# Optimization experiments

Hardware: AMD Instinct MI355X
Metric: run time of the kernel (lower is better)

## Reference

```python
import jax, jax.numpy as jnp
import numpy as np

N_NODES = 100000
N_EDGES = 1600000
N_GRAPHS = 256
D_IN = 128
D_HID = 128
D_OUT = 10
N_GIN_LAYERS = 4  # num_layers - 1
BN_EPS = 1e-5


def setup_inputs() -> dict:
    key = jax.random.key(0)
    ks = jax.random.split(key, 16)
    x = jax.random.normal(ks[0], (N_NODES, D_IN), dtype=jnp.float32)
    edge_src = jax.random.randint(ks[1], (N_EDGES,), 0, N_NODES)
    edge_dst = jax.random.randint(ks[2], (N_EDGES,), 0, N_NODES)
    graph_ids = jnp.sort(jax.random.randint(ks[3], (N_NODES,), 0, N_GRAPHS))
    s = 1.0 / np.sqrt(D_HID)
    # stacked per-layer params (all layers 128->128 since input_dim == hidden_dim)
    W1 = jax.random.normal(ks[4], (N_GIN_LAYERS, D_HID, D_HID), dtype=jnp.float32) * s
    b1 = jnp.zeros((N_GIN_LAYERS, D_HID), dtype=jnp.float32)
    g1 = jnp.ones((N_GIN_LAYERS, D_HID), dtype=jnp.float32)
    bt1 = jnp.zeros((N_GIN_LAYERS, D_HID), dtype=jnp.float32)
    W2 = jax.random.normal(ks[5], (N_GIN_LAYERS, D_HID, D_HID), dtype=jnp.float32) * s
    b2 = jnp.zeros((N_GIN_LAYERS, D_HID), dtype=jnp.float32)
    g2 = jnp.ones((N_GIN_LAYERS, D_HID), dtype=jnp.float32)
    bt2 = jnp.zeros((N_GIN_LAYERS, D_HID), dtype=jnp.float32)
    eps = jnp.zeros((N_GIN_LAYERS,), dtype=jnp.float32)          # learn_eps params
    fusion_w = jnp.ones((N_GIN_LAYERS,), dtype=jnp.float32)      # self.weight
    Wp = jax.random.normal(ks[6], (D_HID, D_OUT), dtype=jnp.float32) * s
    bp = jnp.zeros((D_OUT,), dtype=jnp.float32)
    return {"x": x, "edge_src": edge_src, "edge_dst": edge_dst, "graph_ids": graph_ids,
            "eps": eps, "fusion_w": fusion_w, "W1": W1, "b1": b1, "g1": g1, "bt1": bt1,
            "W2": W2, "b2": b2, "g2": g2, "bt2": bt2, "Wp": Wp, "bp": bp}


def _batchnorm(h, gamma, beta):
    # training-mode BatchNorm1d over node axis
    m = jnp.mean(h, axis=0)
    v = jnp.var(h, axis=0)
    return (h - m) * jax.lax.rsqrt(v + BN_EPS) * gamma + beta


def reference(x, edge_src, edge_dst, graph_ids, eps, fusion_w,
              W1, b1, g1, bt1, W2, b2, g2, bt2, Wp, bp):
    h = x
    hiddens = []
    for l in range(N_GIN_LAYERS):
        # sum neighbor aggregation (spmm with learn_eps -> no self loops in Adj)
        pooled = jax.ops.segment_sum(h[edge_src], edge_dst, num_segments=N_NODES)
        pooled = pooled + (1.0 + eps[l]) * h
        # 2-layer MLP: Linear -> BN -> ReLU -> Linear
        t = jax.nn.relu(_batchnorm(pooled @ W1[l] + b1[l], g1[l], bt1[l]))
        t = t @ W2[l] + b2[l]
        # outer BatchNorm + ReLU
        h = jax.nn.relu(_batchnorm(t, g2[l], bt2[l]))
        hiddens.append(h)
    # attention_global, attention_type == 'weight': weighted sum of 4 hidden scales
    fused = (fusion_w[0] * hiddens[0] + fusion_w[1] * hiddens[1]
             + fusion_w[2] * hiddens[2] + fusion_w[3] * hiddens[3])
    # graph sum pooling (graph_pool spmm) then final linear (dropout = eval identity)
    pooled_g = jax.ops.segment_sum(fused, graph_ids, num_segments=N_GRAPHS)
    return pooled_g @ Wp + bp
```

## Files before the change

kernel.cpp:

```cpp
#include <hip/hip_runtime.h>

#define D 128
#define DOUT 10
#define CT_STRIDE 152

typedef float f32x4 __attribute__((ext_vector_type(4)));
typedef __bf16 bf16x8 __attribute__((ext_vector_type(8)));
typedef unsigned short u16;

__device__ __forceinline__ float bf2f(u16 u) {
    return __uint_as_float(((unsigned int)u) << 16);
}
__device__ __forceinline__ u16 f2bf(float f) {
    unsigned int u = __float_as_uint(f);
    u += 0x7fffu + ((u >> 16) & 1u);
    return (u16)(u >> 16);
}

__global__ void k_zero(float4* __restrict__ p, int n4) {
    int i = blockIdx.x * 256 + threadIdx.x;
    if (i < n4) p[i] = make_float4(0.f, 0.f, 0.f, 0.f);
}

__global__ __launch_bounds__(256) void k_prepw(const float* __restrict__ W1,
                                               const float* __restrict__ W2,
                                               bf16x8* __restrict__ wswz, int L) {
    int b = blockIdx.x >> 3;
    const float* W = (b < L) ? (W1 + (size_t)b * D * D)
                             : (W2 + (size_t)(b - L) * D * D);
    bf16x8* o = wswz + (size_t)b * 2048;
    int idx = ((blockIdx.x & 7) << 8) + threadIdx.x;
    int lane_s = idx & 63;
    int f = idx >> 6;
    int n = ((f >> 2) << 4) | (lane_s & 15);
    int kb = ((f & 3) << 5) | ((lane_s >> 4) << 3);
    bf16x8 fr;
#pragma unroll
    for (int j = 0; j < 8; ++j) fr[j] = (__bf16)W[(kb + j) * D + n];
    o[idx] = fr;
}

__global__ __launch_bounds__(256) void k_hist(const int* __restrict__ dst,
                                              int* __restrict__ cnts, int E, int nb) {
    __shared__ int hist[1024];
    int tid = threadIdx.x;
    for (int i = tid; i < nb; i += 256) hist[i] = 0;
    __syncthreads();
    int e0 = blockIdx.x << 11;
    int e1 = e0 + 2048; if (e1 > E) e1 = E;
    for (int e = e0 + tid; e < e1; e += 256) atomicAdd(&hist[dst[e] >> 7], 1);
    __syncthreads();
    for (int i = tid; i < nb; i += 256) cnts[(blockIdx.x << 10) + i] = hist[i];
}

__global__ __launch_bounds__(256) void k_off(int* __restrict__ cnts,
                                             int* __restrict__ btot,
                                             int nbk, int nb) {
    int wave = threadIdx.x >> 6, lane = threadIdx.x & 63;
    int b = blockIdx.x * 4 + wave;
    if (b >= nb) return;
    int carry = 0;
    for (int base = 0; base < nbk; base += 64) {
        int idx = base + lane;
        int orig = (idx < nbk) ? cnts[(idx << 10) + b] : 0;
        int c = orig;
#pragma unroll
        for (int off = 1; off < 64; off <<= 1) {
            int v = __shfl_up(c, off);
            if (lane >= off) c += v;
        }
        if (idx < nbk) cnts[(idx << 10) + b] = carry + (c - orig);
        carry += __shfl(c, 63);
    }
    if (lane == 0) btot[b] = carry;
}

__global__ __launch_bounds__(256) void k_scat(const int* __restrict__ src,
                                              const int* __restrict__ dst,
                                              const int* __restrict__ cnts,
                                              int* __restrict__ pairs, int E, int nb) {
    __shared__ int lbase[1024];
    __shared__ int lcur[1024];
    int tid = threadIdx.x;
    for (int i = tid; i < nb; i += 256) {
        lbase[i] = cnts[(blockIdx.x << 10) + i];
        lcur[i] = 0;
    }
    __syncthreads();
    int e0 = blockIdx.x << 11;
    int e1 = e0 + 2048; if (e1 > E) e1 = E;
    for (int e = e0 + tid; e < e1; e += 256) {
        int d = dst[e];
        int b = d >> 7;
        int pos = lbase[b] + atomicAdd(&lcur[b], 1);
        if (pos < 4096) pairs[(b << 12) + pos] = (src[e] << 7) | (d & 127);
    }
}

__global__ void k_cvt(const float* __restrict__ x, u16* __restrict__ o,
                      int M, int Mpad) {
    long e = ((long)blockIdx.x * 256 + threadIdx.x) * 4;
    if (e >= (long)Mpad * D) return;
    ushort4 r;
    if (e < (long)M * D) {
        float4 v = *(const float4*)(x + e);
        r.x = f2bf(v.x); r.y = f2bf(v.y); r.z = f2bf(v.z); r.w = f2bf(v.w);
    } else {
        r = make_ushort4(0, 0, 0, 0);
    }
    *(ushort4*)(o + e) = r;
}

__global__ __launch_bounds__(512) void k_agg(
        const u16* __restrict__ h, const int* __restrict__ pairs,
        const int* __restrict__ bcnt, const float* __restrict__ eps, int layer,
        u16* __restrict__ out, int M, int Mpad, int b0) {
    __shared__ int lcnt[128];
    __shared__ int loff[128];
    __shared__ int lcur[128];
    __shared__ int ledge[4096];
    int tid = threadIdx.x;
    if (tid < 128) lcnt[tid] = 0;
    __syncthreads();

    int b = b0 + blockIdx.x;
    int cnt = bcnt[b];
    if (cnt > 4096) cnt = 4096;
    const int* pb = pairs + ((size_t)b << 12);

    for (int e = tid; e < cnt; e += 512)
        atomicAdd(&lcnt[pb[e] & 127], 1);
    __syncthreads();

    if (tid < 128) loff[tid] = lcnt[tid];
    __syncthreads();
    for (int off = 1; off < 128; off <<= 1) {
        int v = 0;
        if (tid < 128 && tid >= off) v = loff[tid - off];
        __syncthreads();
        if (tid < 128) loff[tid] += v;
        __syncthreads();
    }
    if (tid < 128) lcur[tid] = loff[tid] - lcnt[tid];
    __syncthreads();

    for (int e = tid; e < cnt; e += 512) {
        int p = pb[e];
        int pos = atomicAdd(&lcur[p & 127], 1);
        ledge[pos] = p >> 7;
    }
    __syncthreads();

    float e1 = 1.0f + eps[layer];
    int grp = tid >> 5;
    int c = (tid & 31) << 2;
    for (int pass = 0; pass < 8; ++pass) {
        int row = (pass << 4) + grp;
        int node = (b << 7) + row;
        if (node >= Mpad) continue;
        u16* op = out + ((size_t)node << 7) + c;
        if (node >= M) { *(ushort4*)op = make_ushort4(0, 0, 0, 0); continue; }
        ushort4 sv = *(const ushort4*)(h + ((size_t)node << 7) + c);
        float a0 = e1 * bf2f(sv.x), a1 = e1 * bf2f(sv.y);
        float a2 = e1 * bf2f(sv.z), a3 = e1 * bf2f(sv.w);
        int dd = lcnt[row];
        int s = loff[row] - dd;
        int i = 0;
        for (; i + 8 <= dd; i += 8) {
            int n0 = ledge[s + i],     n1 = ledge[s + i + 1];
            int n2 = ledge[s + i + 2], n3 = ledge[s + i + 3];
            int n4 = ledge[s + i + 4], n5 = ledge[s + i + 5];
            int n6 = ledge[s + i + 6], n7 = ledge[s + i + 7];
            ushort4 u0 = *(const ushort4*)(h + ((size_t)n0 << 7) + c);
            ushort4 u1 = *(const ushort4*)(h + ((size_t)n1 << 7) + c);
            ushort4 u2 = *(const ushort4*)(h + ((size_t)n2 << 7) + c);
            ushort4 u3 = *(const ushort4*)(h + ((size_t)n3 << 7) + c);
            ushort4 u4 = *(const ushort4*)(h + ((size_t)n4 << 7) + c);
            ushort4 u5 = *(const ushort4*)(h + ((size_t)n5 << 7) + c);
            ushort4 u6 = *(const ushort4*)(h + ((size_t)n6 << 7) + c);
            ushort4 u7 = *(const ushort4*)(h + ((size_t)n7 << 7) + c);
            a0 += bf2f(u0.x) + bf2f(u1.x) + bf2f(u2.x) + bf2f(u3.x)
                + bf2f(u4.x) + bf2f(u5.x) + bf2f(u6.x) + bf2f(u7.x);
            a1 += bf2f(u0.y) + bf2f(u1.y) + bf2f(u2.y) + bf2f(u3.y)
                + bf2f(u4.y) + bf2f(u5.y) + bf2f(u6.y) + bf2f(u7.y);
            a2 += bf2f(u0.z) + bf2f(u1.z) + bf2f(u2.z) + bf2f(u3.z)
                + bf2f(u4.z) + bf2f(u5.z) + bf2f(u6.z) + bf2f(u7.z);
            a3 += bf2f(u0.w) + bf2f(u1.w) + bf2f(u2.w) + bf2f(u3.w)
                + bf2f(u4.w) + bf2f(u5.w) + bf2f(u6.w) + bf2f(u7.w);
        }
        for (; i + 4 <= dd; i += 4) {
            int n0 = ledge[s + i],     n1 = ledge[s + i + 1];
            int n2 = ledge[s + i + 2], n3 = ledge[s + i + 3];
            ushort4 u0 = *(const ushort4*)(h + ((size_t)n0 << 7) + c);
            ushort4 u1 = *(const ushort4*)(h + ((size_t)n1 << 7) + c);
            ushort4 u2 = *(const ushort4*)(h + ((size_t)n2 << 7) + c);
            ushort4 u3 = *(const ushort4*)(h + ((size_t)n3 << 7) + c);
            a0 += bf2f(u0.x) + bf2f(u1.x) + bf2f(u2.x) + bf2f(u3.x);
            a1 += bf2f(u0.y) + bf2f(u1.y) + bf2f(u2.y) + bf2f(u3.y);
            a2 += bf2f(u0.z) + bf2f(u1.z) + bf2f(u2.z) + bf2f(u3.z);
            a3 += bf2f(u0.w) + bf2f(u1.w) + bf2f(u2.w) + bf2f(u3.w);
        }
        for (; i < dd; ++i) {
            int n0 = ledge[s + i];
            ushort4 u0 = *(const ushort4*)(h + ((size_t)n0 << 7) + c);
            a0 += bf2f(u0.x); a1 += bf2f(u0.y); a2 += bf2f(u0.z); a3 += bf2f(u0.w);
        }
        ushort4 r;
        r.x = f2bf(a0); r.y = f2bf(a1); r.z = f2bf(a2); r.w = f2bf(a3);
        *(ushort4*)op = r;
    }
}

__global__ __launch_bounds__(256, 4) void k_gemm_bf(
        const u16* __restrict__ A, u16* __restrict__ O,
        const bf16x8* __restrict__ wz, const float* __restrict__ bias,
        float* __restrict__ stats, int M) {
    __shared__ union { bf16x8 w[2048]; u16 c[64 * CT_STRIDE]; } sh;
    __shared__ float blds[D], psum[4 * D], psq[4 * D];
    int tid = threadIdx.x;
    int wave = tid >> 6, lane = tid & 63;
    int m = lane & 15, quad = lane >> 4;
    int row0 = blockIdx.x * 64 + wave * 16;

    const u16* ap = A + (size_t)(row0 + m) * D + (quad << 3);
    bf16x8 a[4];
#pragma unroll
    for (int kc = 0; kc < 4; ++kc) a[kc] = *(const bf16x8*)(ap + (kc << 5));

    for (int i = tid; i < 2048; i += 256) sh.w[i] = wz[i];
    if (tid < D) blds[tid] = bias[tid];
    __syncthreads();

    f32x4 z = {0.f, 0.f, 0.f, 0.f};
    f32x4 acc[8];
#pragma unroll
    for (int t = 0; t < 8; ++t) acc[t] = z;

#pragma unroll
    for (int kc = 0; kc < 4; ++kc)
#pragma unroll
        for (int t = 0; t < 8; ++t)
            acc[t] = __builtin_amdgcn_mfma_f32_16x16x32_bf16(
                a[kc], sh.w[(((t << 2) | kc) << 6) | lane], acc[t], 0, 0, 0);
    __syncthreads();

    int lr0 = wave * 16 + (quad << 2);
    int gr0 = blockIdx.x * 64 + lr0;
#pragma unroll
    for (int t = 0; t < 8; ++t) {
        int cch = (t << 4) | m;
        float bc = blds[cch];
        float s = 0.f, q = 0.f;
#pragma unroll
        for (int r = 0; r < 4; ++r) {
            float v = acc[t][r] + bc;
            sh.c[(lr0 + r) * CT_STRIDE + cch] = f2bf(v);
            if (gr0 + r < M) { s += v; q += v * v; }
        }
        s += __shfl_xor(s, 16); s += __shfl_xor(s, 32);
        q += __shfl_xor(q, 16); q += __shfl_xor(q, 32);
        if (quad == 0) { psum[wave * D + cch] = s; psq[wave * D + cch] = q; }
    }
    __syncthreads();

    int mrow = M - blockIdx.x * 64;
#pragma unroll
    for (int i = 0; i < 4; ++i) {
        int idx = (i << 8) + tid;
        int row = idx >> 4, ch8 = (idx & 15) << 3;
        if (row < mrow) {
            float4 v = *(const float4*)&sh.c[row * CT_STRIDE + ch8];
            *(float4*)(O + ((size_t)(blockIdx.x * 64 + row) << 7) + ch8) = v;
        }
    }
    if (tid < D) {
        float s = psum[tid] + psum[D + tid] + psum[2 * D + tid] + psum[3 * D + tid];
        float q = psq[tid] + psq[D + tid] + psq[2 * D + tid] + psq[3 * D + tid];
        float* st = stats + ((blockIdx.x & 7) << 8);
        atomicAdd(&st[tid], s);
        atomicAdd(&st[D + tid], q);
    }
}

__global__ __launch_bounds__(256, 4) void k_gemm_bn(
        u16* __restrict__ A, const bf16x8* __restrict__ wz,
        const float* __restrict__ bias, const float* __restrict__ stats_in,
        const float* __restrict__ gamma, const float* __restrict__ beta,
        float* __restrict__ stats_out, float invM, int M) {
    __shared__ union { bf16x8 w[2048]; u16 c[64 * CT_STRIDE]; } sh;
    __shared__ float blds[D], s_sc[D], s_sh[D], psum[4 * D], psq[4 * D];
    int tid = threadIdx.x;
    int wave = tid >> 6, lane = tid & 63;
    int m = lane & 15, quad = lane >> 4;
    int row0 = blockIdx.x * 64 + wave * 16;

    const u16* ap = A + (size_t)(row0 + m) * D + (quad << 3);
    ushort4 p[4][2];
#pragma unroll
    for (int kc = 0; kc < 4; ++kc) {
        p[kc][0] = *(const ushort4*)(ap + (kc << 5));
        p[kc][1] = *(const ushort4*)(ap + (kc << 5) + 4);
    }

    for (int i = tid; i < 2048; i += 256) sh.w[i] = wz[i];
    if (tid < D) {
        float s = 0.f, q = 0.f;
#pragma unroll
        for (int r = 0; r < 8; ++r) {
            s += stats_in[(r << 8) + tid];
            q += stats_in[(r << 8) + D + tid];
        }
        float mean = s * invM;
        float var = q * invM - mean * mean;
        float sc = rsqrtf(var + 1e-5f) * gamma[tid];
        s_sc[tid] = sc;
        s_sh[tid] = beta[tid] - mean * sc;
        blds[tid] = bias[tid];
    }
    __syncthreads();

    f32x4 z = {0.f, 0.f, 0.f, 0.f};
    f32x4 acc[8];
#pragma unroll
    for (int t = 0; t < 8; ++t) acc[t] = z;

#pragma unroll
    for (int kc = 0; kc < 4; ++kc) {
        int kb = (kc << 5) | (quad << 3);
        float4 c0 = *(const float4*)&s_sc[kb];
        float4 c1 = *(const float4*)&s_sc[kb + 4];
        float4 h0 = *(const float4*)&s_sh[kb];
        float4 h1 = *(const float4*)&s_sh[kb + 4];
        ushort4 p0 = p[kc][0], p1 = p[kc][1];
        bf16x8 af;
        af[0] = (__bf16)fmaxf(0.f, fmaf(bf2f(p0.x), c0.x, h0.x));
        af[1] = (__bf16)fmaxf(0.f, fmaf(bf2f(p0.y), c0.y, h0.y));
        af[2] = (__bf16)fmaxf(0.f, fmaf(bf2f(p0.z), c0.z, h0.z));
        af[3] = (__bf16)fmaxf(0.f, fmaf(bf2f(p0.w), c0.w, h0.w));
        af[4] = (__bf16)fmaxf(0.f, fmaf(bf2f(p1.x), c1.x, h1.x));
        af[5] = (__bf16)fmaxf(0.f, fmaf(bf2f(p1.y), c1.y, h1.y));
        af[6] = (__bf16)fmaxf(0.f, fmaf(bf2f(p1.z), c1.z, h1.z));
        af[7] = (__bf16)fmaxf(0.f, fmaf(bf2f(p1.w), c1.w, h1.w));
#pragma unroll
        for (int t = 0; t < 8; ++t)
            acc[t] = __builtin_amdgcn_mfma_f32_16x16x32_bf16(
                af, sh.w[(((t << 2) | kc) << 6) | lane], acc[t], 0, 0, 0);
    }
    __syncthreads();

    int lr0 = wave * 16 + (quad << 2);
    int gr0 = blockIdx.x * 64 + lr0;
#pragma unroll
    for (int t = 0; t < 8; ++t) {
        int cch = (t << 4) | m;
        float bc = blds[cch];
        float s = 0.f, q = 0.f;
#pragma unroll
        for (int r = 0; r < 4; ++r) {
            float v = acc[t][r] + bc;
            sh.c[(lr0 + r) * CT_STRIDE + cch] = f2bf(v);
            if (gr0 + r < M) { s += v; q += v * v; }
        }
        s += __shfl_xor(s, 16); s += __shfl_xor(s, 32);
        q += __shfl_xor(q, 16); q += __shfl_xor(q, 32);
        if (quad == 0) { psum[wave * D + cch] = s; psq[wave * D + cch] = q; }
    }
    __syncthreads();

    int mrow = M - blockIdx.x * 64;
#pragma unroll
    for (int i = 0; i < 4; ++i) {
        int idx = (i << 8) + tid;
        int row = idx >> 4, ch8 = (idx & 15) << 3;
        if (row < mrow) {
            float4 v = *(const float4*)&sh.c[row * CT_STRIDE + ch8];
            *(float4*)(A + ((size_t)(blockIdx.x * 64 + row) << 7) + ch8) = v;
        }
    }
    if (tid < D) {
        float s = psum[tid] + psum[D + tid] + psum[2 * D + tid] + psum[3 * D + tid];
        float q = psq[tid] + psq[D + tid] + psq[2 * D + tid] + psq[3 * D + tid];
        float* st = stats_out + ((blockIdx.x & 7) << 8);
        atomicAdd(&st[tid], s);
        atomicAdd(&st[D + tid], q);
    }
}

__global__ __launch_bounds__(256) void k_bn2pool(
        const u16* __restrict__ y, const float* __restrict__ stats,
        const float* __restrict__ gamma, const float* __restrict__ beta,
        const int* __restrict__ gids, const float* __restrict__ fw,
        int layer, u16* __restrict__ hout, float* __restrict__ gacc,
        float invM, int M) {
    __shared__ float s_sc[D], s_sh[D];
    int t = threadIdx.x;
    if (t < D) {
        float s = 0.f, q = 0.f;
#pragma unroll
        for (int r = 0; r < 8; ++r) {
            s += stats[(r << 8) + t];
            q += stats[(r << 8) + D + t];
        }
        float mean = s * invM;
        float sv = rsqrtf(q * invM - mean * mean + 1e-5f) * gamma[t];
        s_sc[t] = sv;
        s_sh[t] = beta[t] - mean * sv;
    }
    __syncthreads();

    int c = (t & 31) << 2;
    int strip = t >> 5;
    long base = (long)blockIdx.x * 64 + (long)strip * 8;
    if (base >= M) return;
    float4 sc4 = *(const float4*)&s_sc[c];
    float4 sh4 = *(const float4*)&s_sh[c];

    ushort4 v[8];
#pragma unroll
    for (int r = 0; r < 8; ++r)
        v[r] = *(const ushort4*)(y + ((base + r) << 7) + c);
    long gmax = (long)M - 1;
    int g[8];
#pragma unroll
    for (int r = 0; r < 8; ++r) {
        long idx = base + r;
        g[r] = gids[idx > gmax ? gmax : idx];
    }

    float h0[8], h1[8], h2[8], h3[8];
#pragma unroll
    for (int r = 0; r < 8; ++r) {
        h0[r] = fmaxf(0.f, fmaf(bf2f(v[r].x), sc4.x, sh4.x));
        h1[r] = fmaxf(0.f, fmaf(bf2f(v[r].y), sc4.y, sh4.y));
        h2[r] = fmaxf(0.f, fmaf(bf2f(v[r].z), sc4.z, sh4.z));
        h3[r] = fmaxf(0.f, fmaf(bf2f(v[r].w), sc4.w, sh4.w));
    }
#pragma unroll
    for (int r = 0; r < 8; ++r) {
        if (base + r < M) {
            ushort4 o;
            o.x = f2bf(h0[r]); o.y = f2bf(h1[r]);
            o.z = f2bf(h2[r]); o.w = f2bf(h3[r]);
            *(ushort4*)(hout + ((base + r) << 7) + c) = o;
        }
    }

    float wl = fw[layer];
    int cur = -1;
    float a0 = 0.f, a1 = 0.f, a2 = 0.f, a3 = 0.f;
#pragma unroll
    for (int r = 0; r < 8; ++r) {
        if (base + r < M) {
            if (g[r] != cur) {
                if (cur >= 0) {
                    float* gp = gacc + ((size_t)cur << 7) + c;
                    atomicAdd(gp, wl * a0); atomicAdd(gp + 1, wl * a1);
                    atomicAdd(gp + 2, wl * a2); atomicAdd(gp + 3, wl * a3);
                }
                cur = g[r];
                a0 = a1 = a2 = a3 = 0.f;
            }
            a0 += h0[r]; a1 += h1[r]; a2 += h2[r]; a3 += h3[r];
        }
    }
    if (cur >= 0) {
        float* gp = gacc + ((size_t)cur << 7) + c;
        atomicAdd(gp, wl * a0); atomicAdd(gp + 1, wl * a1);
        atomicAdd(gp + 2, wl * a2); atomicAdd(gp + 3, wl * a3);
    }
}

__global__ void k_final(const float* __restrict__ gacc, const float* __restrict__ Wp,
                        const float* __restrict__ bp, float* __restrict__ out) {
    __shared__ float w[D * DOUT];
    __shared__ float bb[DOUT];
    int t = threadIdx.x;
    for (int i = t; i < D * DOUT; i += blockDim.x) w[i] = Wp[i];
    if (t < DOUT) bb[t] = bp[t];
    __syncthreads();
    float acc[DOUT];
#pragma unroll
    for (int o = 0; o < DOUT; ++o) acc[o] = bb[o];
    for (int k = 0; k < D; ++k) {
        float a = gacc[(size_t)t * D + k];
#pragma unroll
        for (int o = 0; o < DOUT; ++o) acc[o] += a * w[k * DOUT + o];
    }
#pragma unroll
    for (int o = 0; o < DOUT; ++o) out[(size_t)t * DOUT + o] = acc[o];
}

extern "C" void kernel_launch(void* const* d_in, const int* in_sizes, int n_in,
                              void* d_out, int out_size, void* d_ws, size_t ws_size,
                              hipStream_t stream) {
    const float* x    = (const float*)d_in[0];
    const int* esrc   = (const int*)d_in[1];
    const int* edst   = (const int*)d_in[2];
    const int* gids   = (const int*)d_in[3];
    const float* eps  = (const float*)d_in[4];
    const float* fw   = (const float*)d_in[5];
    const float* W1   = (const float*)d_in[6];
    const float* b1   = (const float*)d_in[7];
    const float* g1   = (const float*)d_in[8];
    const float* bt1  = (const float*)d_in[9];
    const float* W2   = (const float*)d_in[10];
    const float* b2   = (const float*)d_in[11];
    const float* g2   = (const float*)d_in[12];
    const float* bt2  = (const float*)d_in[13];
    const float* Wp   = (const float*)d_in[14];
    const float* bp   = (const float*)d_in[15];
    float* out        = (float*)d_out;

    const int M = in_sizes[3];
    const int E = in_sizes[1];
    const int L = in_sizes[4];
    const int G = out_size / DOUT;
    const int nb  = (M + 127) >> 7;
    const int Mpad = nb << 7;
    const int nbk = (E + 2047) >> 11;
    const int nbh = nb >> 1;
    const float invM = 1.0f / (float)M;

    char* ws = (char*)d_ws;
    u16* bufP  = (u16*)ws;  ws += (size_t)Mpad * D * 2;
    u16* bufT  = (u16*)ws;  ws += (size_t)Mpad * D * 2;
    u16* bufH  = (u16*)ws;  ws += (size_t)Mpad * D * 2;
    int* pairs = (int*)ws;  ws += (size_t)nb * 4096 * 4;
    int* cnts  = (int*)ws;  ws += (size_t)nbk * 1024 * 4;
    int* btot  = (int*)ws;  ws += 1024 * 4;
    bf16x8* wswz = (bf16x8*)ws; ws += (size_t)2 * L * 2048 * 16;
    float* stats = (float*)ws; ws += (size_t)L * 4096 * 4;
    float* gacc  = (float*)ws; ws += (size_t)G * D * 4;

    int zbytes = L * 4096 * 4 + G * D * 4;
    int n4 = zbytes / 16;
    k_zero<<<(n4 + 255) / 256, 256, 0, stream>>>((float4*)stats, n4);

    k_prepw<<<2 * L * 8, 256, 0, stream>>>(W1, W2, wswz, L);
    k_hist<<<nbk, 256, 0, stream>>>(edst, cnts, E, nb);
    k_off<<<(nb + 3) / 4, 256, 0, stream>>>(cnts, btot, nbk, nb);
    k_scat<<<nbk, 256, 0, stream>>>(esrc, edst, cnts, pairs, E, nb);
    k_cvt<<<(Mpad * (D / 4) + 255) / 256, 256, 0, stream>>>(x, bufH, M, Mpad);

    int gemm_grid = Mpad / 64;
    int pool_grid = (M + 63) / 64;
    for (int l = 0; l < L; ++l) {
        float* st1 = stats + (size_t)l * 4096;
        float* st2 = st1 + 2048;
        k_agg<<<nbh, 512, 0, stream>>>(bufH, pairs, btot, eps, l, bufP, M, Mpad, 0);
        k_agg<<<nb - nbh, 512, 0, stream>>>(bufH, pairs, btot, eps, l, bufP, M, Mpad, nbh);
        k_gemm_bf<<<gemm_grid, 256, 0, stream>>>(bufP, bufT, wswz + (size_t)l * 2048,
                                                 b1 + (size_t)l * D, st1, M);
        k_gemm_bn<<<gemm_grid, 256, 0, stream>>>(bufT, wswz + (size_t)(L + l) * 2048,
                                                 b2 + (size_t)l * D, st1,
                                                 g1 + (size_t)l * D, bt1 + (size_t)l * D,
                                                 st2, invM, M);
        k_bn2pool<<<pool_grid, 256, 0, stream>>>(bufT, st2, g2 + (size_t)l * D,
                                                 bt2 + (size_t)l * D, gids, fw, l,
                                                 bufH, gacc, invM, M);
    }
    k_final<<<1, G, 0, stream>>>(gacc, Wp, bp, out);
}
```

Baseline: 766.2 us.

## Fuse neighbor aggregation with first MLP GEMM in one kernel

The aggregation kernel now keeps its 128-row aggregated tile in shared memory and runs the first linear layer (MFMA), bias add and BN statistics accumulation in the same block. This removes the intermediate bufP round trip through global memory and one kernel launch per layer. In exchange the fused kernel uses more LDS (weights, tile and 8-wave partial stats) and more registers for the per-pass results, which may lower occupancy during the latency-bound gather phase.

```diff
diff --git a/kernel.cpp b/kernel.cpp
--- a/kernel.cpp
+++ b/kernel.cpp
@@ -3,6 +3,7 @@
 #define D 128
 #define DOUT 10
 #define CT_STRIDE 152
+#define TSTR 136
 
 typedef float f32x4 __attribute__((ext_vector_type(4)));
 typedef __bf16 bf16x8 __attribute__((ext_vector_type(8)));
@@ -111,16 +112,22 @@
     *(ushort4*)(o + e) = r;
 }
 
-__global__ __launch_bounds__(512) void k_agg(
+__global__ __launch_bounds__(512, 4) void k_aggemm(
         const u16* __restrict__ h, const int* __restrict__ pairs,
         const int* __restrict__ bcnt, const float* __restrict__ eps, int layer,
-        u16* __restrict__ out, int M, int Mpad, int b0) {
-    __shared__ int lcnt[128];
-    __shared__ int loff[128];
-    __shared__ int lcur[128];
-    __shared__ int ledge[4096];
+        const bf16x8* __restrict__ wz, const float* __restrict__ bias,
+        u16* __restrict__ O, float* __restrict__ stats, int M, int b0) {
+    __shared__ union UA {
+        struct { int lcnt[128]; int loff[128]; int lcur[128]; int ledge[4096]; } csr;
+        u16 tile[128 * TSTR];
+    } shA;
+    __shared__ bf16x8 shW[2048];
+    __shared__ float blds[D], psum[8 * D], psq[8 * D];
     int tid = threadIdx.x;
-    if (tid < 128) lcnt[tid] = 0;
+
+    if (tid < 128) shA.csr.lcnt[tid] = 0;
+    for (int i = tid; i < 2048; i += 512) shW[i] = wz[i];
+    if (tid < D) blds[tid] = bias[tid];
     __syncthreads();
 
     int b = b0 + blockIdx.x;
@@ -129,123 +136,113 @@
     const int* pb = pairs + ((size_t)b << 12);
 
     for (int e = tid; e < cnt; e += 512)
-        atomicAdd(&lcnt[pb[e] & 127], 1);
-    __syncthreads();
-
-    if (tid < 128) loff[tid] = lcnt[tid];
+        atomicAdd(&shA.csr.lcnt[pb[e] & 127], 1);
+    __syncthreads();
+    if (tid < 128) shA.csr.loff[tid] = shA.csr.lcnt[tid];
     __syncthreads();
     for (int off = 1; off < 128; off <<= 1) {
         int v = 0;
-        if (tid < 128 && tid >= off) v = loff[tid - off];
+        if (tid < 128 && tid >= off) v = shA.csr.loff[tid - off];
         __syncthreads();
-        if (tid < 128) loff[tid] += v;
+        if (tid < 128) shA.csr.loff[tid] += v;
         __syncthreads();
     }
-    if (tid < 128) lcur[tid] = loff[tid] - lcnt[tid];
-    __syncthreads();
-
+    if (tid < 128) shA.csr.lcur[tid] = shA.csr.loff[tid] - shA.csr.lcnt[tid];
+    __syncthreads();
     for (int e = tid; e < cnt; e += 512) {
         int p = pb[e];
-        int pos = atomicAdd(&lcur[p & 127], 1);
-        ledge[pos] = p >> 7;
+        int pos = atomicAdd(&shA.csr.lcur[p & 127], 1);
+        shA.csr.ledge[pos] = p >> 7;
     }
     __syncthreads();
 
     float e1 = 1.0f + eps[layer];
     int grp = tid >> 5;
     int c = (tid & 31) << 2;
+    float r0[8], r1[8], r2[8], r3[8];
     for (int pass = 0; pass < 8; ++pass) {
         int row = (pass << 4) + grp;
         int node = (b << 7) + row;
-        if (node >= Mpad) continue;
-        u16* op = out + ((size_t)node << 7) + c;
-        if (node >= M) { *(ushort4*)op = make_ushort4(0, 0, 0, 0); continue; }
-        ushort4 sv = *(const ushort4*)(h + ((size_t)node << 7) + c);
-        float a0 = e1 * bf2f(sv.x), a1 = e1 * bf2f(sv.y);
-        float a2 = e1 * bf2f(sv.z), a3 = e1 * bf2f(sv.w);
-        int dd = lcnt[row];
-        int s = loff[row] - dd;
-        int i = 0;
-        for (; i + 8 <= dd; i += 8) {
-            int n0 = ledge[s + i],     n1 = ledge[s + i + 1];
-            int n2 = ledge[s + i + 2], n3 = ledge[s + i + 3];
-            int n4 = ledge[s + i + 4], n5 = ledge[s + i + 5];
-            int n6 = ledge[s + i + 6], n7 = ledge[s + i + 7];
-            ushort4 u0 = *(const ushort4*)(h + ((size_t)n0 << 7) + c);
-            ushort4 u1 = *(const ushort4*)(h + ((size_t)n1 << 7) + c);
-            ushort4 u2 = *(const ushort4*)(h + ((size_t)n2 << 7) + c);
-            ushort4 u3 = *(const ushort4*)(h + ((size_t)n3 << 7) + c);
-            ushort4 u4 = *(const ushort4*)(h + ((size_t)n4 << 7) + c);
-            ushort4 u5 = *(const ushort4*)(h + ((size_t)n5 << 7) + c);
-            ushort4 u6 = *(const ushort4*)(h + ((size_t)n6 << 7) + c);
-            ushort4 u7 = *(const ushort4*)(h + ((size_t)n7 << 7) + c);
-            a0 += bf2f(u0.x) + bf2f(u1.x) + bf2f(u2.x) + bf2f(u3.x)
-                + bf2f(u4.x) + bf2f(u5.x) + bf2f(u6.x) + bf2f(u7.x);
-            a1 += bf2f(u0.y) + bf2f(u1.y) + bf2f(u2.y) + bf2f(u3.y)
-                + bf2f(u4.y) + bf2f(u5.y) + bf2f(u6.y) + bf2f(u7.y);
-            a2 += bf2f(u0.z) + bf2f(u1.z) + bf2f(u2.z) + bf2f(u3.z)
-                + bf2f(u4.z) + bf2f(u5.z) + bf2f(u6.z) + bf2f(u7.z);
-            a3 += bf2f(u0.w) + bf2f(u1.w) + bf2f(u2.w) + bf2f(u3.w)
-                + bf2f(u4.w) + bf2f(u5.w) + bf2f(u6.w) + bf2f(u7.w);
-        }
-        for (; i + 4 <= dd; i += 4) {
-            int n0 = ledge[s + i],     n1 = ledge[s + i + 1];
-            int n2 = ledge[s + i + 2], n3 = ledge[s + i + 3];
-            ushort4 u0 = *(const ushort4*)(h + ((size_t)n0 << 7) + c);
-            ushort4 u1 = *(const ushort4*)(h + ((size_t)n1 << 7) + c);
-            ushort4 u2 = *(const ushort4*)(h + ((size_t)n2 << 7) + c);
-            ushort4 u3 = *(const ushort4*)(h + ((size_t)n3 << 7) + c);
-            a0 += bf2f(u0.x) + bf2f(u1.x) + bf2f(u2.x) + bf2f(u3.x);
-            a1 += bf2f(u0.y) + bf2f(u1.y) + bf2f(u2.y) + bf2f(u3.y);
-            a2 += bf2f(u0.z) + bf2f(u1.z) + bf2f(u2.z) + bf2f(u3.z);
-            a3 += bf2f(u0.w) + bf2f(u1.w) + bf2f(u2.w) + bf2f(u3.w);
-        }
-        for (; i < dd; ++i) {
-            int n0 = ledge[s + i];
-            ushort4 u0 = *(const ushort4*)(h + ((size_t)n0 << 7) + c);
-            a0 += bf2f(u0.x); a1 += bf2f(u0.y); a2 += bf2f(u0.z); a3 += bf2f(u0.w);
-        }
-        ushort4 r;
-        r.x = f2bf(a0); r.y = f2bf(a1); r.z = f2bf(a2); r.w = f2bf(a3);
-        *(ushort4*)op = r;
-    }
-}
-
-__global__ __launch_bounds__(256, 4) void k_gemm_bf(
-        const u16* __restrict__ A, u16* __restrict__ O,
-        const bf16x8* __restrict__ wz, const float* __restrict__ bias,
-        float* __restrict__ stats, int M) {
-    __shared__ union { bf16x8 w[2048]; u16 c[64 * CT_STRIDE]; } sh;
-    __shared__ float blds[D], psum[4 * D], psq[4 * D];
-    int tid = threadIdx.x;
+        float a0 = 0.f, a1 = 0.f, a2 = 0.f, a3 = 0.f;
+        if (node < M) {
+            ushort4 sv = *(const ushort4*)(h + ((size_t)node << 7) + c);
+            a0 = e1 * bf2f(sv.x); a1 = e1 * bf2f(sv.y);
+            a2 = e1 * bf2f(sv.z); a3 = e1 * bf2f(sv.w);
+            int dd = shA.csr.lcnt[row];
+            int s = shA.csr.loff[row] - dd;
+            int i = 0;
+            for (; i + 8 <= dd; i += 8) {
+                int n0 = shA.csr.ledge[s + i],     n1 = shA.csr.ledge[s + i + 1];
+                int n2 = shA.csr.ledge[s + i + 2], n3 = shA.csr.ledge[s + i + 3];
+                int n4 = shA.csr.ledge[s + i + 4], n5 = shA.csr.ledge[s + i + 5];
+                int n6 = shA.csr.ledge[s + i + 6], n7 = shA.csr.ledge[s + i + 7];
+                ushort4 u0 = *(const ushort4*)(h + ((size_t)n0 << 7) + c);
+                ushort4 u1 = *(const ushort4*)(h + ((size_t)n1 << 7) + c);
+                ushort4 u2 = *(const ushort4*)(h + ((size_t)n2 << 7) + c);
+                ushort4 u3 = *(const ushort4*)(h + ((size_t)n3 << 7) + c);
+                ushort4 u4 = *(const ushort4*)(h + ((size_t)n4 << 7) + c);
+                ushort4 u5 = *(const ushort4*)(h + ((size_t)n5 << 7) + c);
+                ushort4 u6 = *(const ushort4*)(h + ((size_t)n6 << 7) + c);
+                ushort4 u7 = *(const ushort4*)(h + ((size_t)n7 << 7) + c);
+                a0 += bf2f(u0.x) + bf2f(u1.x) + bf2f(u2.x) + bf2f(u3.x)
+                    + bf2f(u4.x) + bf2f(u5.x) + bf2f(u6.x) + bf2f(u7.x);
+                a1 += bf2f(u0.y) + bf2f(u1.y) + bf2f(u2.y) + bf2f(u3.y)
+                    + bf2f(u4.y) + bf2f(u5.y) + bf2f(u6.y) + bf2f(u7.y);
+                a2 += bf2f(u0.z) + bf2f(u1.z) + bf2f(u2.z) + bf2f(u3.z)
+                    + bf2f(u4.z) + bf2f(u5.z) + bf2f(u6.z) + bf2f(u7.z);
+                a3 += bf2f(u0.w) + bf2f(u1.w) + bf2f(u2.w) + bf2f(u3.w)
+                    + bf2f(u4.w) + bf2f(u5.w) + bf2f(u6.w) + bf2f(u7.w);
+            }
+            for (; i + 4 <= dd; i += 4) {
+                int n0 = shA.csr.ledge[s + i],     n1 = shA.csr.ledge[s + i + 1];
+                int n2 = shA.csr.ledge[s + i + 2], n3 = shA.csr.ledge[s + i + 3];
+                ushort4 u0 = *(const ushort4*)(h + ((size_t)n0 << 7) + c);
+                ushort4 u1 = *(const ushort4*)(h + ((size_t)n1 << 7) + c);
+                ushort4 u2 = *(const ushort4*)(h + ((size_t)n2 << 7) + c);
+                ushort4 u3 = *(const ushort4*)(h + ((size_t)n3 << 7) + c);
+                a0 += bf2f(u0.x) + bf2f(u1.x) + bf2f(u2.x) + bf2f(u3.x);
+                a1 += bf2f(u0.y) + bf2f(u1.y) + bf2f(u2.y) + bf2f(u3.y);
+                a2 += bf2f(u0.z) + bf2f(u1.z) + bf2f(u2.z) + bf2f(u3.z);
+                a3 += bf2f(u0.w) + bf2f(u1.w) + bf2f(u2.w) + bf2f(u3.w);
+            }
+            for (; i < dd; ++i) {
+                int n0 = shA.csr.ledge[s + i];
+                ushort4 u0 = *(const ushort4*)(h + ((size_t)n0 << 7) + c);
+                a0 += bf2f(u0.x); a1 += bf2f(u0.y); a2 += bf2f(u0.z); a3 += bf2f(u0.w);
+            }
+        }
+        r0[pass] = a0; r1[pass] = a1; r2[pass] = a2; r3[pass] = a3;
+    }
+    __syncthreads();
+
+#pragma unroll
+    for (int pass = 0; pass < 8; ++pass) {
+        int row = (pass << 4) + grp;
+        ushort4 v;
+        v.x = f2bf(r0[pass]); v.y = f2bf(r1[pass]);
+        v.z = f2bf(r2[pass]); v.w = f2bf(r3[pass]);
+        *(ushort4*)&shA.tile[row * TSTR + c] = v;
+    }
+    __syncthreads();
+
     int wave = tid >> 6, lane = tid & 63;
     int m = lane & 15, quad = lane >> 4;
-    int row0 = blockIdx.x * 64 + wave * 16;
-
-    const u16* ap = A + (size_t)(row0 + m) * D + (quad << 3);
-    bf16x8 a[4];
-#pragma unroll
-    for (int kc = 0; kc < 4; ++kc) a[kc] = *(const bf16x8*)(ap + (kc << 5));
-
-    for (int i = tid; i < 2048; i += 256) sh.w[i] = wz[i];
-    if (tid < D) blds[tid] = bias[tid];
-    __syncthreads();
-
     f32x4 z = {0.f, 0.f, 0.f, 0.f};
     f32x4 acc[8];
 #pragma unroll
     for (int t = 0; t < 8; ++t) acc[t] = z;
-
-#pragma unroll
-    for (int kc = 0; kc < 4; ++kc)
+#pragma unroll
+    for (int kc = 0; kc < 4; ++kc) {
+        bf16x8 af = *(const bf16x8*)&shA.tile[(wave * 16 + m) * TSTR + (kc << 5) + (quad << 3)];
 #pragma unroll
         for (int t = 0; t < 8; ++t)
             acc[t] = __builtin_amdgcn_mfma_f32_16x16x32_bf16(
-                a[kc], sh.w[(((t << 2) | kc) << 6) | lane], acc[t], 0, 0, 0);
+                af, shW[(((t << 2) | kc) << 6) | lane], acc[t], 0, 0, 0);
+    }
     __syncthreads();
 
     int lr0 = wave * 16 + (quad << 2);
-    int gr0 = blockIdx.x * 64 + lr0;
+    int gr0 = (b << 7) + lr0;
 #pragma unroll
     for (int t = 0; t < 8; ++t) {
         int cch = (t << 4) | m;
@@ -254,7 +251,7 @@
 #pragma unroll
         for (int r = 0; r < 4; ++r) {
             float v = acc[t][r] + bc;
-            sh.c[(lr0 + r) * CT_STRIDE + cch] = f2bf(v);
+            shA.tile[(lr0 + r) * TSTR + cch] = f2bf(v);
             if (gr0 + r < M) { s += v; q += v * v; }
         }
         s += __shfl_xor(s, 16); s += __shfl_xor(s, 32);
@@ -263,20 +260,21 @@
     }
     __syncthreads();
 
-    int mrow = M - blockIdx.x * 64;
+    int mrow = M - (b << 7);
 #pragma unroll
     for (int i = 0; i < 4; ++i) {
-        int idx = (i << 8) + tid;
+        int idx = (i << 9) + tid;
         int row = idx >> 4, ch8 = (idx & 15) << 3;
         if (row < mrow) {
-            float4 v = *(const float4*)&sh.c[row * CT_STRIDE + ch8];
-            *(float4*)(O + ((size_t)(blockIdx.x * 64 + row) << 7) + ch8) = v;
+            float4 v = *(const float4*)&shA.tile[row * TSTR + ch8];
+            *(float4*)(O + (((size_t)(b << 7) + row) << 7) + ch8) = v;
         }
     }
     if (tid < D) {
-        float s = psum[tid] + psum[D + tid] + psum[2 * D + tid] + psum[3 * D + tid];
-        float q = psq[tid] + psq[D + tid] + psq[2 * D + tid] + psq[3 * D + tid];
-        float* st = stats + ((blockIdx.x & 7) << 8);
+        float s = 0.f, q = 0.f;
+#pragma unroll
+        for (int w = 0; w < 8; ++w) { s += psum[w * D + tid]; q += psq[w * D + tid]; }
+        float* st = stats + ((b & 7) << 8);
         atomicAdd(&st[tid], s);
         atomicAdd(&st[D + tid], q);
     }
@@ -522,7 +520,6 @@
     const float invM = 1.0f / (float)M;
 
     char* ws = (char*)d_ws;
-    u16* bufP  = (u16*)ws;  ws += (size_t)Mpad * D * 2;
     u16* bufT  = (u16*)ws;  ws += (size_t)Mpad * D * 2;
     u16* bufH  = (u16*)ws;  ws += (size_t)Mpad * D * 2;
     int* pairs = (int*)ws;  ws += (size_t)nb * 4096 * 4;
@@ -542,16 +539,17 @@
     k_scat<<<nbk, 256, 0, stream>>>(esrc, edst, cnts, pairs, E, nb);
     k_cvt<<<(Mpad * (D / 4) + 255) / 256, 256, 0, stream>>>(x, bufH, M, Mpad);
 
-    int gemm_grid = Mpad / 64;
     int pool_grid = (M + 63) / 64;
     for (int l = 0; l < L; ++l) {
         float* st1 = stats + (size_t)l * 4096;
         float* st2 = st1 + 2048;
-        k_agg<<<nbh, 512, 0, stream>>>(bufH, pairs, btot, eps, l, bufP, M, Mpad, 0);
-        k_agg<<<nb - nbh, 512, 0, stream>>>(bufH, pairs, btot, eps, l, bufP, M, Mpad, nbh);
-        k_gemm_bf<<<gemm_grid, 256, 0, stream>>>(bufP, bufT, wswz + (size_t)l * 2048,
-                                                 b1 + (size_t)l * D, st1, M);
-        k_gemm_bn<<<gemm_grid, 256, 0, stream>>>(bufT, wswz + (size_t)(L + l) * 2048,
+        k_aggemm<<<nbh, 512, 0, stream>>>(bufH, pairs, btot, eps, l,
+                                          wswz + (size_t)l * 2048, b1 + (size_t)l * D,
+                                          bufT, st1, M, 0);
+        k_aggemm<<<nb - nbh, 512, 0, stream>>>(bufH, pairs, btot, eps, l,
+                                               wswz + (size_t)l * 2048, b1 + (size_t)l * D,
+                                               bufT, st1, M, nbh);
+        k_gemm_bn<<<Mpad / 64, 256, 0, stream>>>(bufT, wswz + (size_t)(L + l) * 2048,
                                                  b2 + (size_t)l * D, st1,
                                                  g1 + (size_t)l * D, bt1 + (size_t)l * D,
                                                  st2, invM, M);
```

After: 745.3 us. 1.03x faster.
